# Kernel tuning notes

Hardware: AMD Instinct MI355X
Metric: run time of the kernel (lower is better)

The kernel has to match this reference:

```python
import jax, jax.numpy as jnp
import numpy as np
from jax import lax

STRIDE = 2
PAD = 1
KT = 3   # conv_transpose kernel
KP = 6   # fused pool window/stride (2*3)

def setup_inputs() -> dict:
    key = jax.random.key(0)
    kx, kw, kb = jax.random.split(key, 3)
    x = jax.random.normal(kx, (8, 32, 32, 32, 32), dtype=jnp.float32)
    W = jax.random.normal(kw, (32, 16, KT, KT, KT), dtype=jnp.float32) * 0.05
    b = jax.random.normal(kb, (16,), dtype=jnp.float32) * 0.05
    return {"x": x, "W": W, "b": b}

def _conv_transpose3d(x, W, b):
    # PyTorch conv_transpose3d: weight (C_in, C_out, k, k, k)
    # equivalent to conv with lhs dilation, flipped kernel, swapped I/O axes
    w2 = jnp.flip(W, axis=(2, 3, 4)).swapaxes(0, 1)  # (C_out, C_in, k, k, k)
    pad = KT - 1 - PAD
    y = lax.conv_general_dilated(
        x, w2,
        window_strides=(1, 1, 1),
        padding=[(pad, pad)] * 3,
        lhs_dilation=(STRIDE, STRIDE, STRIDE),
        dimension_numbers=("NCDHW", "OIDHW", "NCDHW"),
    )
    return y + b[None, :, None, None, None]

def reference(x, W, b):
    y = _conv_transpose3d(x, W, b)  # (N, C_out, 63, 63, 63)
    # fused maxpool(k=2,s=2) + maxpool(k=3,s=3) == maxpool(k=6,s=6)
    pooled = lax.reduce_window(
        y, -jnp.inf, lax.max,
        window_dimensions=(1, 1, KP, KP, KP),
        window_strides=(1, 1, KP, KP, KP),
        padding="VALID",
    )  # (N, C_out, 10, 10, 10)
    return jnp.sum(pooled, axis=1, keepdims=True)  # (N, 1, 10, 10, 10)
```

## Files before the change

kernel.cpp:

```cpp
#include <hip/hip_runtime.h>

typedef __bf16 bf16;
typedef __bf16 bf16x8 __attribute__((ext_vector_type(8)));
typedef float f32x4 __attribute__((ext_vector_type(4)));

#define W_STRIDE 40
#define H_STRIDE (33 * W_STRIDE)
#define D_STRIDE (5 * H_STRIDE)
#define XS_ELEMS (4 * D_STRIDE)

__global__ void transpose_w_kernel(const float* __restrict__ W, bf16* __restrict__ Wt) {
  int o = blockIdx.x * 256 + threadIdx.x;
  if (o < 27 * 512) {
    int j = o & 7, co = (o >> 3) & 15, q = (o >> 7) & 3, tap = o >> 9;
    Wt[o] = (bf16)W[((q * 8 + j) * 16 + co) * 27 + tap];
  }
}

__global__ __launch_bounds__(256) void fused_mfma_kernel(
    const float* __restrict__ x, const bf16* __restrict__ Wt,
    const float* __restrict__ b, float* __restrict__ out) {
  __shared__ __align__(16) bf16 xs[XS_ELEMS];
  __shared__ float red[10][2][16];

  const int t = threadIdx.x;
  const int lane = t & 63;
  const int wv = t >> 6;
  const int co = lane & 15;
  const int quad = lane >> 4;

  const int blk = blockIdx.x;
  const int n = blk / 100;
  const int od = (blk / 10) % 10;
  const int oh = blk % 10;

  bf16x8 bfrag[27];
  {
    const bf16x8* wp = (const bf16x8*)Wt;
#pragma unroll
    for (int tap = 0; tap < 27; ++tap)
      bfrag[tap] = wp[(tap * 4 + quad) * 16 + co];
  }

  {
    const float* xn = x + (size_t)n * (32 * 32768) + (3 * od) * 1024 + (3 * oh) * 32;
#pragma unroll 2
    for (int it = 0; it < 8; ++it) {
      const int flat = it * 256 + t;
      const int w = flat & 31;
      const int row = flat >> 5;
      const int cig = row & 3;
      const int lh = (row >> 2) & 3;
      const int ld = row >> 4;
      const float* g = xn + (size_t)(cig * 8) * 32768 + ld * 1024 + lh * 32 + w;
      bf16x8 pk;
#pragma unroll
      for (int j = 0; j < 8; ++j) pk[j] = (bf16)g[(size_t)j * 32768];
      *(bf16x8*)&xs[ld * D_STRIDE + lh * H_STRIDE + w * W_STRIDE + cig * 8] = pk;
    }
  }
  __syncthreads();

  const int tile = wv >> 1;
  const int tb = tile * 16;
  int pos = tb + (lane & 15);
  if (pos > 26) pos = 26;
  const int md = pos / 9;
  const int mh = (pos / 3) % 3;
  const int mw = pos % 3;

  for (int i = 0; i < 5; ++i) {
    const int w10 = (wv & 1) * 5 + i;
    const bf16* ap = xs + md * D_STRIDE + mh * H_STRIDE + (3 * w10 + mw) * W_STRIDE + quad * 8;

    bf16x8 af[8];
#pragma unroll
    for (int dd = 0; dd < 2; ++dd)
#pragma unroll
      for (int dh = 0; dh < 2; ++dh)
#pragma unroll
        for (int dw = 0; dw < 2; ++dw)
          af[dd * 4 + dh * 2 + dw] =
              *(const bf16x8*)(ap + dd * D_STRIDE + dh * H_STRIDE + dw * W_STRIDE);

    float tmax = -3.4e38f;
#pragma unroll
    for (int pd = 0; pd < 2; ++pd)
#pragma unroll
      for (int ph = 0; ph < 2; ++ph)
#pragma unroll
        for (int pw = 0; pw < 2; ++pw) {
          f32x4 acc = {0.f, 0.f, 0.f, 0.f};
#pragma unroll
          for (int td = 0; td <= pd; ++td)
#pragma unroll
            for (int th = 0; th <= ph; ++th)
#pragma unroll
              for (int tw = 0; tw <= pw; ++tw) {
                const int kd = pd ? (td ? 2 : 0) : 1;
                const int kh = ph ? (th ? 2 : 0) : 1;
                const int kw = pw ? (tw ? 2 : 0) : 1;
                const int ai = ((kd == 0) ? 4 : 0) + ((kh == 0) ? 2 : 0) + ((kw == 0) ? 1 : 0);
                acc = __builtin_amdgcn_mfma_f32_16x16x32_bf16(
                    af[ai], bfrag[kd * 9 + kh * 3 + kw], acc, 0, 0, 0);
              }
          if (tile == 0) {
#pragma unroll
            for (int r = 0; r < 4; ++r) tmax = fmaxf(tmax, acc[r]);
          } else {
#pragma unroll
            for (int r = 0; r < 4; ++r)
              if (16 + quad * 4 + r < 27) tmax = fmaxf(tmax, acc[r]);
          }
        }

    tmax = fmaxf(tmax, __shfl_xor(tmax, 16, 64));
    tmax = fmaxf(tmax, __shfl_xor(tmax, 32, 64));
    if (quad == 0) red[w10][tile][co] = tmax;
  }
  __syncthreads();

  if (t < 160) {
    const int w10 = t >> 4;
    const int c = t & 15;
    float v = fmaxf(red[w10][0][c], red[w10][1][c]) + b[c];
    v += __shfl_xor(v, 1, 64);
    v += __shfl_xor(v, 2, 64);
    v += __shfl_xor(v, 4, 64);
    v += __shfl_xor(v, 8, 64);
    if (c == 0) out[blk * 10 + w10] = v;
  }
}

extern "C" void kernel_launch(void* const* d_in, const int* in_sizes, int n_in,
                              void* d_out, int out_size, void* d_ws, size_t ws_size,
                              hipStream_t stream) {
  const float* x = (const float*)d_in[0];
  const float* W = (const float*)d_in[1];
  const float* b = (const float*)d_in[2];
  float* out = (float*)d_out;
  bf16* Wt = (bf16*)d_ws;

  transpose_w_kernel<<<dim3(54), dim3(256), 0, stream>>>(W, Wt);
  fused_mfma_kernel<<<dim3(800), dim3(256), 0, stream>>>(x, Wt, b, out);
}
```

Before: 92.19 us.

## Drop weight-transpose kernel, vectorize x loads, interleave batch in block order

Removes the separate weight transpose launch and has each thread gather and convert its weight fragments from the fp32 weights directly. The x tile load is rewritten so each thread issues 16-byte float4 global loads over 8 channels and writes four packed bf16x8 vectors to shared memory, replacing scalar loads. Block indexing is changed so consecutive blocks take different batch items, and the output index is recomputed to match. The per-thread weight gather is strided and repeated in every block, which adds scattered global reads in exchange for dropping one launch.

```diff
diff --git a/kernel.cpp b/kernel.cpp
--- a/kernel.cpp
+++ b/kernel.cpp
@@ -9,16 +9,8 @@
 #define D_STRIDE (5 * H_STRIDE)
 #define XS_ELEMS (4 * D_STRIDE)
 
-__global__ void transpose_w_kernel(const float* __restrict__ W, bf16* __restrict__ Wt) {
-  int o = blockIdx.x * 256 + threadIdx.x;
-  if (o < 27 * 512) {
-    int j = o & 7, co = (o >> 3) & 15, q = (o >> 7) & 3, tap = o >> 9;
-    Wt[o] = (bf16)W[((q * 8 + j) * 16 + co) * 27 + tap];
-  }
-}
-
 __global__ __launch_bounds__(256) void fused_mfma_kernel(
-    const float* __restrict__ x, const bf16* __restrict__ Wt,
+    const float* __restrict__ x, const float* __restrict__ W,
     const float* __restrict__ b, float* __restrict__ out) {
   __shared__ __align__(16) bf16 xs[XS_ELEMS];
   __shared__ float red[10][2][16];
@@ -30,40 +22,48 @@
   const int quad = lane >> 4;
 
   const int blk = blockIdx.x;
-  const int n = blk / 100;
-  const int od = (blk / 10) % 10;
-  const int oh = blk % 10;
+  const int n = blk & 7;
+  const int odoh = blk >> 3;
+  const int od = odoh / 10;
+  const int oh = odoh % 10;
+
+  {
+    const float* xn = x + (size_t)n * (32 * 32768) + (3 * od) * 1024 + (3 * oh) * 32;
+#pragma unroll
+    for (int it = 0; it < 2; ++it) {
+      const int f = it * 256 + t;
+      const int wg = f & 7;
+      const int cig = (f >> 3) & 3;
+      const int lh = (f >> 5) & 3;
+      const int ld = f >> 7;
+      const float* g = xn + (size_t)(cig * 8) * 32768 + ld * 1024 + lh * 32 + wg * 4;
+      f32x4 v[8];
+#pragma unroll
+      for (int j = 0; j < 8; ++j) v[j] = *(const f32x4*)(g + (size_t)j * 32768);
+      bf16* base = &xs[ld * D_STRIDE + lh * H_STRIDE + (wg * 4) * W_STRIDE + cig * 8];
+#pragma unroll
+      for (int k = 0; k < 4; ++k) {
+        bf16x8 pk;
+#pragma unroll
+        for (int j = 0; j < 8; ++j) pk[j] = (bf16)v[j][k];
+        *(bf16x8*)(base + k * W_STRIDE) = pk;
+      }
+    }
+  }
 
   bf16x8 bfrag[27];
   {
-    const bf16x8* wp = (const bf16x8*)Wt;
 #pragma unroll
-    for (int tap = 0; tap < 27; ++tap)
-      bfrag[tap] = wp[(tap * 4 + quad) * 16 + co];
-  }
-
-  {
-    const float* xn = x + (size_t)n * (32 * 32768) + (3 * od) * 1024 + (3 * oh) * 32;
-#pragma unroll 2
-    for (int it = 0; it < 8; ++it) {
-      const int flat = it * 256 + t;
-      const int w = flat & 31;
-      const int row = flat >> 5;
-      const int cig = row & 3;
-      const int lh = (row >> 2) & 3;
-      const int ld = row >> 4;
-      const float* g = xn + (size_t)(cig * 8) * 32768 + ld * 1024 + lh * 32 + w;
-      bf16x8 pk;
+    for (int j = 0; j < 8; ++j) {
+      const float* wr = W + ((quad * 8 + j) * 16 + co) * 27;
 #pragma unroll
-      for (int j = 0; j < 8; ++j) pk[j] = (bf16)g[(size_t)j * 32768];
-      *(bf16x8*)&xs[ld * D_STRIDE + lh * H_STRIDE + w * W_STRIDE + cig * 8] = pk;
+      for (int tap = 0; tap < 27; ++tap) bfrag[tap][j] = (bf16)wr[tap];
     }
   }
   __syncthreads();
 
   const int tile = wv >> 1;
-  const int tb = tile * 16;
-  int pos = tb + (lane & 15);
+  int pos = tile * 16 + (lane & 15);
   if (pos > 26) pos = 26;
   const int md = pos / 9;
   const int mh = (pos / 3) % 3;
@@ -128,7 +128,7 @@
     v += __shfl_xor(v, 2, 64);
     v += __shfl_xor(v, 4, 64);
     v += __shfl_xor(v, 8, 64);
-    if (c == 0) out[blk * 10 + w10] = v;
+    if (c == 0) out[n * 1000 + od * 100 + oh * 10 + w10] = v;
   }
 }
 
@@ -139,8 +139,5 @@
   const float* W = (const float*)d_in[1];
   const float* b = (const float*)d_in[2];
   float* out = (float*)d_out;
-  bf16* Wt = (bf16*)d_ws;
-
-  transpose_w_kernel<<<dim3(54), dim3(256), 0, stream>>>(W, Wt);
-  fused_mfma_kernel<<<dim3(800), dim3(256), 0, stream>>>(x, Wt, b, out);
+  fused_mfma_kernel<<<dim3(800), dim3(256), 0, stream>>>(x, W, b, out);
 }
```

Measured after the change: 108.5 us. 1.18x slower.
